# Optimization experiments

Measured on AMD Instinct MI355X. Metric: run time of the kernel, lower is better.

## Reference

```python
import jax, jax.numpy as jnp
import numpy as np

B, T, C, H = 8, 2048, 1024, 64  # batch, seq, n_embed, head_size


def setup_inputs() -> dict:
    key = jax.random.key(0)
    ks = jax.random.split(key, 6)
    k = jax.random.normal(ks[0], (B, T, C), dtype=jnp.float32)
    q = jax.random.normal(ks[1], (B, T, C), dtype=jnp.float32)
    v = jax.random.normal(ks[2], (B, T, C), dtype=jnp.float32)
    mask = jnp.ones((B, T), dtype=jnp.int32)  # key-padding mask (1 = keep)
    # nn.Linear(n_embed, head_size, bias=False) weights: [head_size, n_embed]
    s = 1.0 / np.sqrt(C)
    Wk = jax.random.uniform(ks[3], (H, C), jnp.float32, -s, s)
    Wq = jax.random.uniform(ks[4], (H, C), jnp.float32, -s, s)
    Wv = jax.random.uniform(ks[5], (H, C), jnp.float32, -s, s)
    return {"k": k, "q": q, "v": v, "mask": mask, "Wk": Wk, "Wq": Wq, "Wv": Wv}


def reference(k, q, v, mask, Wk, Wq, Wv):
    Tq = q.shape[1]
    kh = jnp.einsum('btc,hc->bth', k, Wk)   # [B,T,H]
    qh = jnp.einsum('btc,hc->bth', q, Wq)   # [B,T,H]
    vh = jnp.einsum('btc,hc->bth', v, Wv)   # [B,T,H]
    scale = kh.shape[-1] ** -0.5
    wei = jnp.einsum('bqh,bkh->bqk', qh, kh) * scale  # [B,T,T]
    # causal (tril) mask
    tril = jnp.tril(jnp.ones((Tq, Tq), dtype=bool))
    neg_inf = jnp.finfo(wei.dtype).min
    wei = jnp.where(tril[None, :, :], wei, neg_inf)
    # key-padding mask: mask [B,T] -> broadcast over query rows
    wei = jnp.where(mask[:, None, :] != 0, wei, neg_inf)
    wei = jax.nn.softmax(wei, axis=-1)
    # dropout p=0.0 (eval) -> identity
    out = jnp.einsum('bqk,bkh->bqh', wei, vh)  # [B,T,H]
    return out
```

## Files before the change

### kernel.cpp

```cpp
#include <hip/hip_runtime.h>
#include <hip/hip_bf16.h>
#include <math.h>

#define Bn 8
#define Tn 2048
#define Cn 1024
#define Hn 64
#define BTHb ((size_t)Bn * Tn * Hn)
#define WELEMS ((size_t)Hn * Cn)

typedef __attribute__((ext_vector_type(8))) short bf16x8;
typedef __attribute__((ext_vector_type(4))) float f32x4;

static __device__ __forceinline__ unsigned short bf16rne(float f) {
    union { float f; unsigned u; } x; x.f = f;
    return (unsigned short)((x.u + 0x7FFFu + ((x.u >> 16) & 1u)) >> 16);
}

__global__ __launch_bounds__(256) void wconv_kernel(
    const float* __restrict__ Wk, const float* __restrict__ Wq,
    const float* __restrict__ Wv, unsigned short* __restrict__ dst)
{
    const int g = blockIdx.x * 256 + threadIdx.x;
    const float* src = (g < 16384) ? Wk : (g < 32768) ? Wq : Wv;
    const int local = g & 16383;
    const float4 f = ((const float4*)src)[local];
    ushort4 u;
    u.x = bf16rne(f.x); u.y = bf16rne(f.y);
    u.z = bf16rne(f.z); u.w = bf16rne(f.w);
    ((ushort4*)dst)[g] = u;
}

__global__ __launch_bounds__(256) void proj_kernel(
    const float* __restrict__ k, const float* __restrict__ q,
    const float* __restrict__ v,
    unsigned short* __restrict__ ws)
{
    const int which = blockIdx.y;
    const float* X = (which == 0) ? k : (which == 1) ? q : v;
    const unsigned short* Wsrc = ws + 3 * BTHb + (size_t)which * WELEMS;
    unsigned short* O = ws + (size_t)which * BTHb;

    __shared__ unsigned short Wt[64][136];

    const int tid  = threadIdx.x;
    const int wave = __builtin_amdgcn_readfirstlane(tid >> 6);
    const int lane = tid & 63;
    const int ln   = lane & 15;
    const int quad = lane >> 4;
    const int row0 = blockIdx.x * 64;

    const int wrow = tid >> 2;
    const int wseg = tid & 3;

    const float* Xrow = X + (size_t)(row0 + wave * 16 + ln) * Cn + quad * 8;

    f32x4 acc[4];
#pragma unroll
    for (int t = 0; t < 4; ++t) acc[t] = (f32x4){0.f, 0.f, 0.f, 0.f};

    uint4  wreg[4];
    float4 xr[8];

    {
        const uint4* wp =
            (const uint4*)(Wsrc + (size_t)wrow * Cn + wseg * 32);
#pragma unroll
        for (int u = 0; u < 4; ++u) wreg[u] = wp[u];
    }
#pragma unroll
    for (int kc = 0; kc < 4; ++kc) {
        xr[2 * kc]     = *(const float4*)(Xrow + kc * 32);
        xr[2 * kc + 1] = *(const float4*)(Xrow + kc * 32 + 4);
    }

    for (int ct = 0; ct < 8; ++ct) {
        __syncthreads();
        {
            uint4* wd = (uint4*)&Wt[wrow][wseg * 32];
#pragma unroll
            for (int u = 0; u < 4; ++u) wd[u] = wreg[u];
        }
        __syncthreads();

        if (ct < 7) {
            const uint4* wp = (const uint4*)(Wsrc + (size_t)wrow * Cn
                                             + (ct + 1) * 128 + wseg * 32);
#pragma unroll
            for (int u = 0; u < 4; ++u) wreg[u] = wp[u];
        }

        bf16x8 af[4];
#pragma unroll
        for (int kc = 0; kc < 4; ++kc) {
            union { bf16x8 v; unsigned short s[8]; } u;
            const float4 a = xr[2 * kc], b = xr[2 * kc + 1];
            u.s[0] = bf16rne(a.x); u.s[1] = bf16rne(a.y);
            u.s[2] = bf16rne(a.z); u.s[3] = bf16rne(a.w);
            u.s[4] = bf16rne(b.x); u.s[5] = bf16rne(b.y);
            u.s[6] = bf16rne(b.z); u.s[7] = bf16rne(b.w);
            af[kc] = u.v;
        }

        if (ct < 7) {
#pragma unroll
            for (int kc = 0; kc < 4; ++kc) {
                xr[2 * kc]     = *(const float4*)(Xrow + (ct + 1) * 128
                                                  + kc * 32);
                xr[2 * kc + 1] = *(const float4*)(Xrow + (ct + 1) * 128
                                                  + kc * 32 + 4);
            }
        }

#pragma unroll
        for (int kc = 0; kc < 4; ++kc) {
#pragma unroll
            for (int ht = 0; ht < 4; ++ht) {
                const bf16x8 bfr =
                    *(const bf16x8*)&Wt[ht * 16 + ln][kc * 32 + quad * 8];
                acc[ht] = __builtin_amdgcn_mfma_f32_16x16x32_bf16(
                    af[kc], bfr, acc[ht], 0, 0, 0);
            }
        }
    }

#pragma unroll
    for (int ht = 0; ht < 4; ++ht)
#pragma unroll
        for (int r = 0; r < 4; ++r)
            O[(size_t)(row0 + wave * 16 + quad * 4 + r) * Hn + ht * 16 + ln] =
                bf16rne(acc[ht][r]);
}

__global__ __launch_bounds__(256) void attn_kernel(
    const unsigned short* __restrict__ ws,
    const int* __restrict__ mask,
    float* __restrict__ out)
{
    const unsigned short* kh = ws;
    const unsigned short* qh = ws + BTHb;
    const unsigned short* vh = ws + 2 * BTHb;

    const int b   = blockIdx.y;
    const int qt  = blockIdx.x;
    const int tid = threadIdx.x;
    const int wave = __builtin_amdgcn_readfirstlane(tid >> 6);
    const int lane = tid & 63;
    const int ln   = lane & 15;
    const int quad = lane >> 4;

    __shared__ unsigned short Ks[64][72];
    __shared__ unsigned short Vt[64][72];
    __shared__ unsigned short Ps[64][72];
    __shared__ int Msk[64];

    const int wrb = qt * 64 + wave * 16;

    bf16x8 qa[2];
#pragma unroll
    for (int kc = 0; kc < 2; ++kc)
        qa[kc] = *(const bf16x8*)(qh + ((size_t)b * Tn + wrb + ln) * Hn
                                     + kc * 32 + quad * 8);

    f32x4 oacc[4];
#pragma unroll
    for (int t = 0; t < 4; ++t) oacc[t] = (f32x4){0.f, 0.f, 0.f, 0.f};
    float mrow[4] = {-1e30f, -1e30f, -1e30f, -1e30f};
    float lrow[4] = {0.f, 0.f, 0.f, 0.f};

    const int krow = tid >> 2, kseg = tid & 3;
    const int vcol = tid & 63, vseg = tid >> 6;

    uint4 kreg[2], vreg[2];
    int mreg = 0;
    {
        const unsigned short* kp =
            kh + ((size_t)b * Tn + krow) * Hn + kseg * 16;
        kreg[0] = *(const uint4*)kp;
        kreg[1] = *(const uint4*)(kp + 8);
        const unsigned short* vp =
            vh + ((size_t)b * Tn + vcol) * Hn + vseg * 16;
        vreg[0] = *(const uint4*)vp;
        vreg[1] = *(const uint4*)(vp + 8);
        if (tid < 64) mreg = mask[(size_t)b * Tn + tid];
    }

    for (int j = 0; j <= qt; ++j) {
        __syncthreads();
        *(uint4*)&Ks[krow][kseg * 16]     = kreg[0];
        *(uint4*)&Ks[krow][kseg * 16 + 8] = kreg[1];
        {
            const unsigned short* vs = (const unsigned short*)vreg;
#pragma unroll
            for (int jj = 0; jj < 16; ++jj)
                Vt[vseg * 16 + jj][vcol] = vs[jj];
        }
        if (tid < 64) Msk[tid] = mreg;
        __syncthreads();

        if (j < qt) {
            const unsigned short* kp =
                kh + ((size_t)b * Tn + (j + 1) * 64 + krow) * Hn + kseg * 16;
            kreg[0] = *(const uint4*)kp;
            kreg[1] = *(const uint4*)(kp + 8);
            const unsigned short* vp =
                vh + ((size_t)b * Tn + (j + 1) * 64 + vcol) * Hn + vseg * 16;
            vreg[0] = *(const uint4*)vp;
            vreg[1] = *(const uint4*)(vp + 8);
            if (tid < 64) mreg = mask[(size_t)b * Tn + (j + 1) * 64 + tid];
        }

        f32x4 sacc[4];
#pragma unroll
        for (int t = 0; t < 4; ++t) sacc[t] = (f32x4){0.f, 0.f, 0.f, 0.f};
#pragma unroll
        for (int kc = 0; kc < 2; ++kc) {
#pragma unroll
            for (int nt = 0; nt < 4; ++nt) {
                const bf16x8 kb =
                    *(const bf16x8*)&Ks[nt * 16 + ln][kc * 32 + quad * 8];
                sacc[nt] = __builtin_amdgcn_mfma_f32_16x16x32_bf16(
                    qa[kc], kb, sacc[nt], 0, 0, 0);
            }
        }

        const bool fullv = (j < qt);
        float pv[4][4];
        float mt[4] = {-1e30f, -1e30f, -1e30f, -1e30f};
#pragma unroll
        for (int nt = 0; nt < 4; ++nt) {
            const bool mk = (Msk[nt * 16 + ln] != 0);
            const int kpos = j * 64 + nt * 16 + ln;
#pragma unroll
            for (int r = 0; r < 4; ++r) {
                float s = sacc[nt][r] * 0.125f;
                const bool valid =
                    mk && (fullv || kpos <= wrb + quad * 4 + r);
                s = valid ? s : -1e30f;
                pv[nt][r] = s;
                mt[r] = fmaxf(mt[r], s);
            }
        }
#pragma unroll
        for (int r = 0; r < 4; ++r) {
            mt[r] = fmaxf(mt[r], __shfl_xor(mt[r], 1));
            mt[r] = fmaxf(mt[r], __shfl_xor(mt[r], 2));
            mt[r] = fmaxf(mt[r], __shfl_xor(mt[r], 4));
            mt[r] = fmaxf(mt[r], __shfl_xor(mt[r], 8));
        }
        float alpha[4], rsum[4];
#pragma unroll
        for (int r = 0; r < 4; ++r) {
            const float mn = fmaxf(mrow[r], mt[r]);
            alpha[r] = __expf(mrow[r] - mn);
            mrow[r] = mn;
            rsum[r] = 0.f;
        }
#pragma unroll
        for (int nt = 0; nt < 4; ++nt)
#pragma unroll
            for (int r = 0; r < 4; ++r) {
                const float p = (pv[nt][r] <= -1e29f)
                                    ? 0.f
                                    : __expf(pv[nt][r] - mrow[r]);
                pv[nt][r] = p;
                rsum[r] += p;
            }
#pragma unroll
        for (int r = 0; r < 4; ++r) {
            rsum[r] += __shfl_xor(rsum[r], 1);
            rsum[r] += __shfl_xor(rsum[r], 2);
            rsum[r] += __shfl_xor(rsum[r], 4);
            rsum[r] += __shfl_xor(rsum[r], 8);
            lrow[r] = lrow[r] * alpha[r] + rsum[r];
        }
#pragma unroll
        for (int nt = 0; nt < 4; ++nt)
#pragma unroll
            for (int r = 0; r < 4; ++r) oacc[nt][r] *= alpha[r];

#pragma unroll
        for (int nt = 0; nt < 4; ++nt)
#pragma unroll
            for (int r = 0; r < 4; ++r)
                Ps[wave * 16 + quad * 4 + r][nt * 16 + ln] =
                    bf16rne(pv[nt][r]);
        asm volatile("s_waitcnt lgkmcnt(0)" ::: "memory");

#pragma unroll
        for (int kc = 0; kc < 2; ++kc) {
            const bf16x8 pa =
                *(const bf16x8*)&Ps[wave * 16 + ln][kc * 32 + quad * 8];
#pragma unroll
            for (int nt = 0; nt < 4; ++nt) {
                const bf16x8 vb =
                    *(const bf16x8*)&Vt[nt * 16 + ln][kc * 32 + quad * 8];
                oacc[nt] = __builtin_amdgcn_mfma_f32_16x16x32_bf16(
                    pa, vb, oacc[nt], 0, 0, 0);
            }
        }
    }

#pragma unroll
    for (int r = 0; r < 4; ++r) {
        const float inv = 1.0f / lrow[r];
        const size_t rowoff = ((size_t)b * Tn + wrb + quad * 4 + r) * Hn;
#pragma unroll
        for (int nt = 0; nt < 4; ++nt)
            out[rowoff + nt * 16 + ln] = oacc[nt][r] * inv;
    }
}

extern "C" void kernel_launch(void* const* d_in, const int* in_sizes, int n_in,
                              void* d_out, int out_size, void* d_ws, size_t ws_size,
                              hipStream_t stream)
{
    const float* k    = (const float*)d_in[0];
    const float* q    = (const float*)d_in[1];
    const float* v    = (const float*)d_in[2];
    const int*   mask = (const int*)d_in[3];
    const float* Wk   = (const float*)d_in[4];
    const float* Wq   = (const float*)d_in[5];
    const float* Wv   = (const float*)d_in[6];
    float* out = (float*)d_out;
    unsigned short* ws = (unsigned short*)d_ws;

    wconv_kernel<<<dim3(192), dim3(256), 0, stream>>>(Wk, Wq, Wv,
                                                      ws + 3 * BTHb);

    dim3 pb(256), pg(Bn * Tn / 64, 3);
    proj_kernel<<<pg, pb, 0, stream>>>(k, q, v, ws);

    dim3 ab(256), ag(Tn / 64, Bn);
    attn_kernel<<<ag, ab, 0, stream>>>(ws, mask, out);
}
```

Measured before the change: 298.0 us.

## Read projection weights directly from global memory and double-buffer X loads

Removes the shared-memory staging of the bf16 weight tile and the two block barriers per chunk. Each wave now loads its weight MFMA fragments straight from global memory, relying on L1/L2 caching since all blocks read the same small weight matrix. X loads are double-buffered in registers with a ping-pong scheme. A launch bound of 2 blocks per CU is also added. The risks are extra global load traffic and latency on weight reads, and higher register pressure from the two X buffers. The last iteration also issues one redundant wrapped-around prefetch.

```diff
diff --git a/kernel.cpp b/kernel.cpp
--- a/kernel.cpp
+++ b/kernel.cpp
@@ -31,7 +31,7 @@
     ((ushort4*)dst)[g] = u;
 }
 
-__global__ __launch_bounds__(256) void proj_kernel(
+__global__ __launch_bounds__(256, 2) void proj_kernel(
     const float* __restrict__ k, const float* __restrict__ q,
     const float* __restrict__ v,
     unsigned short* __restrict__ ws)
@@ -41,8 +41,6 @@
     const unsigned short* Wsrc = ws + 3 * BTHb + (size_t)which * WELEMS;
     unsigned short* O = ws + (size_t)which * BTHb;
 
-    __shared__ unsigned short Wt[64][136];
-
     const int tid  = threadIdx.x;
     const int wave = __builtin_amdgcn_readfirstlane(tid >> 6);
     const int lane = tid & 63;
@@ -50,51 +48,35 @@
     const int quad = lane >> 4;
     const int row0 = blockIdx.x * 64;
 
-    const int wrow = tid >> 2;
-    const int wseg = tid & 3;
-
     const float* Xrow = X + (size_t)(row0 + wave * 16 + ln) * Cn + quad * 8;
+    const unsigned short* Wrow0 = Wsrc + (size_t)(0 * 16 + ln) * Cn + quad * 8;
+    const unsigned short* Wrow1 = Wsrc + (size_t)(1 * 16 + ln) * Cn + quad * 8;
+    const unsigned short* Wrow2 = Wsrc + (size_t)(2 * 16 + ln) * Cn + quad * 8;
+    const unsigned short* Wrow3 = Wsrc + (size_t)(3 * 16 + ln) * Cn + quad * 8;
 
     f32x4 acc[4];
 #pragma unroll
     for (int t = 0; t < 4; ++t) acc[t] = (f32x4){0.f, 0.f, 0.f, 0.f};
 
-    uint4  wreg[4];
-    float4 xr[8];
-
-    {
-        const uint4* wp =
-            (const uint4*)(Wsrc + (size_t)wrow * Cn + wseg * 32);
-#pragma unroll
-        for (int u = 0; u < 4; ++u) wreg[u] = wp[u];
-    }
+    float4 xA[8], xB[8];
+
 #pragma unroll
     for (int kc = 0; kc < 4; ++kc) {
-        xr[2 * kc]     = *(const float4*)(Xrow + kc * 32);
-        xr[2 * kc + 1] = *(const float4*)(Xrow + kc * 32 + 4);
-    }
-
+        xA[2 * kc]     = *(const float4*)(Xrow + kc * 32);
+        xA[2 * kc + 1] = *(const float4*)(Xrow + kc * 32 + 4);
+    }
+
+#pragma unroll 2
     for (int ct = 0; ct < 8; ++ct) {
-        __syncthreads();
-        {
-            uint4* wd = (uint4*)&Wt[wrow][wseg * 32];
-#pragma unroll
-            for (int u = 0; u < 4; ++u) wd[u] = wreg[u];
-        }
-        __syncthreads();
-
-        if (ct < 7) {
-            const uint4* wp = (const uint4*)(Wsrc + (size_t)wrow * Cn
-                                             + (ct + 1) * 128 + wseg * 32);
-#pragma unroll
-            for (int u = 0; u < 4; ++u) wreg[u] = wp[u];
-        }
+        float4* xcur = (ct & 1) ? xB : xA;
+        float4* xnxt = (ct & 1) ? xA : xB;
+        const int ctn = (ct + 1) & 7;
 
         bf16x8 af[4];
 #pragma unroll
         for (int kc = 0; kc < 4; ++kc) {
             union { bf16x8 v; unsigned short s[8]; } u;
-            const float4 a = xr[2 * kc], b = xr[2 * kc + 1];
+            const float4 a = xcur[2 * kc], b = xcur[2 * kc + 1];
             u.s[0] = bf16rne(a.x); u.s[1] = bf16rne(a.y);
             u.s[2] = bf16rne(a.z); u.s[3] = bf16rne(a.w);
             u.s[4] = bf16rne(b.x); u.s[5] = bf16rne(b.y);
@@ -102,25 +84,27 @@
             af[kc] = u.v;
         }
 
-        if (ct < 7) {
-#pragma unroll
-            for (int kc = 0; kc < 4; ++kc) {
-                xr[2 * kc]     = *(const float4*)(Xrow + (ct + 1) * 128
-                                                  + kc * 32);
-                xr[2 * kc + 1] = *(const float4*)(Xrow + (ct + 1) * 128
-                                                  + kc * 32 + 4);
-            }
-        }
-
 #pragma unroll
         for (int kc = 0; kc < 4; ++kc) {
-#pragma unroll
-            for (int ht = 0; ht < 4; ++ht) {
-                const bf16x8 bfr =
-                    *(const bf16x8*)&Wt[ht * 16 + ln][kc * 32 + quad * 8];
-                acc[ht] = __builtin_amdgcn_mfma_f32_16x16x32_bf16(
-                    af[kc], bfr, acc[ht], 0, 0, 0);
-            }
+            xnxt[2 * kc]     = *(const float4*)(Xrow + ctn * 128 + kc * 32);
+            xnxt[2 * kc + 1] = *(const float4*)(Xrow + ctn * 128 + kc * 32 + 4);
+        }
+
+#pragma unroll
+        for (int kc = 0; kc < 4; ++kc) {
+            const int co = ct * 128 + kc * 32;
+            const bf16x8 w0 = *(const bf16x8*)(Wrow0 + co);
+            const bf16x8 w1 = *(const bf16x8*)(Wrow1 + co);
+            const bf16x8 w2 = *(const bf16x8*)(Wrow2 + co);
+            const bf16x8 w3 = *(const bf16x8*)(Wrow3 + co);
+            acc[0] = __builtin_amdgcn_mfma_f32_16x16x32_bf16(af[kc], w0,
+                                                             acc[0], 0, 0, 0);
+            acc[1] = __builtin_amdgcn_mfma_f32_16x16x32_bf16(af[kc], w1,
+                                                             acc[1], 0, 0, 0);
+            acc[2] = __builtin_amdgcn_mfma_f32_16x16x32_bf16(af[kc], w2,
+                                                             acc[2], 0, 0, 0);
+            acc[3] = __builtin_amdgcn_mfma_f32_16x16x32_bf16(af[kc], w3,
+                                                             acc[3], 0, 0, 0);
         }
     }
 
```

Result: no change. 298.4 us (+0.1%).
